# Kernel optimization log

Hardware: AMD Instinct MI355X
Metric: run time of the kernel (lower is better)

The kernel has to match this reference:

```python
import jax, jax.numpy as jnp
import numpy as np

R_S, R_C, P, L, NVOX, CH = 48, 144, 27, 2, 128, 128


def encode(x, L=L):
    # NeRF-style positional encoding: [sin(2^l x), cos(2^l x)] for l in range(L)
    feats = []
    for l in range(L):
        f = (2.0 ** l) * x
        feats.append(jnp.sin(f))
        feats.append(jnp.cos(f))
    return jnp.concatenate(feats, axis=-1)


def setup_inputs() -> dict:
    key = jax.random.key(0)
    ks = jax.random.split(key, 8)
    Np = 524288
    xyz = jax.random.uniform(ks[0], (Np, 3), dtype=jnp.float32)          # inside bbox [0,1]^3
    directions = jax.random.normal(ks[1], (Np, 3), dtype=jnp.float32)
    # voxel grid buffer: linspace over bbox per axis -> (3, NVOX)
    voxel = jnp.stack([jnp.linspace(0.0, 1.0, NVOX)] * 3, axis=0).astype(jnp.float32)
    sigma = 0.1 * jax.random.normal(ks[2], (3, R_S, NVOX), dtype=jnp.float32)
    feature = 0.1 * jax.random.normal(ks[3], (3, R_C, NVOX), dtype=jnp.float32)
    B = jax.random.normal(ks[4], (R_C, P), dtype=jnp.float32)
    din = (P + 3) * L * 2  # 120
    W1 = jax.random.normal(ks[5], (din, CH), dtype=jnp.float32) / jnp.sqrt(din)
    b1 = jnp.zeros((CH,), jnp.float32)
    W2 = jax.random.normal(ks[6], (CH, CH), dtype=jnp.float32) / jnp.sqrt(CH)
    b2 = jnp.zeros((CH,), jnp.float32)
    W3 = jax.random.normal(ks[7], (CH, 3), dtype=jnp.float32) / jnp.sqrt(CH)
    b3 = jnp.zeros((3,), jnp.float32)
    return {"xyz": xyz, "directions": directions, "voxel": voxel, "sigma": sigma,
            "feature": feature, "B": B, "W1": W1, "b1": b1, "W2": W2, "b2": b2,
            "W3": W3, "b3": b3}


def reference(xyz, directions, voxel, sigma, feature, B, W1, b1, W2, b2, W3, b3):
    SIGMA_BIAS = -5.0
    x = xyz.T  # (3, Np)
    Nv = voxel.shape[1]
    # snap_to_voxels: per-axis searchsorted + clamp + gather of grid coords
    inds = jax.vmap(jnp.searchsorted)(voxel, x)           # (3, Np)
    il = jnp.clip(inds - 1, 0, Nv - 1)
    ir = jnp.clip(inds, 0, Nv - 1)
    vl = jnp.take_along_axis(voxel, il, axis=1)           # (3, Np)
    vr = jnp.take_along_axis(voxel, ir, axis=1)
    w = (x - vl) / (vr - vl + 1e-6)                       # (3, Np) lerp weights

    # density: gather (3,R_s,Np), lerp, prod over axes(xyz), sum over rank
    sl = jnp.take_along_axis(sigma, il[:, None, :], axis=2)
    sr = jnp.take_along_axis(sigma, ir[:, None, :], axis=2)
    s = sl + (sr - sl) * w[:, None, :]                    # (3, R_s, Np)
    sigmas = jnp.sum(jnp.prod(s, axis=0), axis=0)         # (Np,)
    sigmas = jax.nn.softplus(sigmas + SIGMA_BIAS)

    # features: same pattern on (3,R_c,Np), then small matmul with B
    fl = jnp.take_along_axis(feature, il[:, None, :], axis=2)
    fr = jnp.take_along_axis(feature, ir[:, None, :], axis=2)
    f = fl + (fr - fl) * w[:, None, :]                    # (3, R_c, Np)
    feats = jnp.einsum('rn,rp->np', jnp.prod(f, axis=0), B)  # (Np, P)

    h = jnp.concatenate([encode(feats, L), encode(directions, L)], axis=1)  # (Np, 120)
    h = jax.nn.leaky_relu(h @ W1 + b1, negative_slope=0.01)
    h = jax.nn.leaky_relu(h @ W2 + b2, negative_slope=0.01)
    rgb = jax.nn.sigmoid(h @ W3 + b3)                     # (Np, 3)
    return sigmas, rgb
```

## Files before the change

### kernel.cpp

```cpp
#include <hip/hip_runtime.h>
#include <cstdint>

constexpr int RS  = 48;
constexpr int RC  = 144;
constexpr int PP  = 27;
constexpr int NV  = 128;
constexpr int CHN = 128;

constexpr int SIG_E  = 0;
constexpr int FEAT_E = 24576;
constexpr int BF_E   = 86016;
constexpr int W1_E   = 91136;
constexpr int W2_E   = 107520;
constexpr int W3_E   = 123904;
constexpr int TOT_E  = 125952;

typedef __attribute__((ext_vector_type(8))) short short8;
typedef __attribute__((ext_vector_type(4))) float f32x4;
typedef __attribute__((ext_vector_type(2))) unsigned int u32x2;
typedef __attribute__((ext_vector_type(4))) unsigned int u32x4;

__device__ __forceinline__ short f2bf(float f) {
    unsigned int u = __builtin_bit_cast(unsigned int, f);
    u += 0x7fffu + ((u >> 16) & 1u);
    return (short)(u >> 16);
}
__device__ __forceinline__ float bfu(unsigned int u) {
    return __builtin_bit_cast(float, u);
}
__device__ __forceinline__ unsigned int pk2bf(float a, float b) {
    unsigned short ua = __builtin_bit_cast(unsigned short, (__bf16)a);
    unsigned short ub = __builtin_bit_cast(unsigned short, (__bf16)b);
    return (unsigned int)ua | ((unsigned int)ub << 16);
}

__global__ void prep_kernel(const float* __restrict__ sigma, const float* __restrict__ feature,
                            const float* __restrict__ Bm, const float* __restrict__ W1,
                            const float* __restrict__ W2, const float* __restrict__ W3,
                            short* __restrict__ ws) {
    int idx = blockIdx.x * 256 + threadIdx.x;
    if (idx >= TOT_E) return;
    float val = 0.f;
    if (idx < FEAT_E) {
        int a = idx / 8192, t = idx % 8192;
        int v = t / 64, r = t % 64;
        val = (r < RS) ? sigma[(a * RS + r) * NV + v] : 0.f;
    } else if (idx < BF_E) {
        int j = idx - FEAT_E;
        int a = j / 20480, t = j % 20480;
        int v = t / 160, r = t % 160;
        val = (r < RC) ? feature[(a * RC + r) * NV + v] : 0.f;
    } else if (idx < W1_E) {
        int j = idx - BF_E;
        int frag = j >> 9, li = (j >> 3) & 63, e = j & 7;
        int kt = frag >> 1, nt = frag & 1;
        int k = kt * 32 + (li >> 4) * 8 + e;
        int n = nt * 16 + (li & 15);
        val = (k < RC && n < PP) ? Bm[k * PP + n] : 0.f;
    } else if (idx < W2_E) {
        int j = idx - W1_E;
        int frag = j >> 9, li = (j >> 3) & 63, e = j & 7;
        int kt = frag >> 3, nt = frag & 7;
        int kn = kt * 32 + (li >> 4) * 8 + e;
        int n = nt * 16 + (li & 15);
        if (kn < 120) {
            int ko;
            if (kn < 108) { ko = (kn & 3) * PP + (kn >> 2); }
            else { int t2 = kn - 108; ko = 108 + (t2 & 3) * 3 + (t2 >> 2); }
            val = W1[ko * CHN + n];
        }
    } else if (idx < W3_E) {
        int j = idx - W2_E;
        int frag = j >> 9, li = (j >> 3) & 63, e = j & 7;
        int kt = frag >> 3, nt = frag & 7;
        int k = kt * 32 + (li >> 4) * 8 + e;
        int n = nt * 16 + (li & 15);
        val = W2[k * CHN + n];
    } else {
        int j = idx - W3_E;
        int frag = j >> 9, li = (j >> 3) & 63, e = j & 7;
        int kt = frag;
        int k = kt * 32 + (li >> 4) * 8 + e;
        int n = li & 15;
        val = (n < 3) ? W3[k * 3 + n] : 0.f;
    }
    ws[idx] = f2bf(val);
}

__device__ __forceinline__ void lerp8(const short* rl, int stride, float w, float* pr, bool first) {
    u32x4 Lo = *(const u32x4*)rl;
    u32x4 Hi = *(const u32x4*)(rl + stride);
#pragma unroll
    for (int d = 0; d < 4; ++d) {
        unsigned int lw = Lo[d], hw = Hi[d];
        float fl0 = bfu(lw << 16), fl1 = bfu(lw & 0xffff0000u);
        float fh0 = bfu(hw << 16), fh1 = bfu(hw & 0xffff0000u);
        float s0 = fmaf(fh0 - fl0, w, fl0);
        float s1 = fmaf(fh1 - fl1, w, fl1);
        if (first) { pr[2 * d] = s0; pr[2 * d + 1] = s1; }
        else       { pr[2 * d] *= s0; pr[2 * d + 1] *= s1; }
    }
}

__global__ __launch_bounds__(256, 8)
void tensorf_main(const float* __restrict__ xyz, const float* __restrict__ dird,
                  const float* __restrict__ voxel,
                  const float* __restrict__ b1, const float* __restrict__ b2,
                  const float* __restrict__ b3,
                  const short* __restrict__ ws, float* __restrict__ out, int Np) {
    __shared__ float voxs[3 * NV];
    __shared__ char  X[4 * 16 * 256];

    const int tid = threadIdx.x;
    const int wid = tid >> 6;
    const int lane = tid & 63;
    const int quad = lane >> 4, lane16 = lane & 15;
    const int wavebase = blockIdx.x * 64 + wid * 16;
    char* Xw = X + wid * 16 * 256;

    for (int i = tid; i < 3 * NV; i += 256) voxs[i] = voxel[i];
    __syncthreads();

    const short* SIGT  = ws + SIG_E;
    const short* FEATT = ws + FEAT_E;
    const short* BFr   = ws + BF_E;

    {
        const int p = wavebase + lane16;

        int ipb[3]; float we[3];
#pragma unroll
        for (int a = 0; a < 3; ++a) {
            float x = xyz[p * 3 + a];
            int ind = (int)ceilf(x * 127.f);
            ind = min(max(ind, 0), 128);
            while (ind > 0 && voxs[a * NV + ind - 1] >= x) --ind;
            while (ind < 128 && voxs[a * NV + ind] < x) ++ind;
            int il = min(max(ind - 1, 0), 127);
            int ir = min(ind, 127);
            float vl = voxs[a * NV + il], vr = voxs[a * NV + ir];
            float w = (x - vl) / (vr - vl + 1e-6f);
            we[a] = (il == 127) ? 1.f : w;
            ipb[a] = min(il, 126);
        }

        float sig = 0.f;
#pragma unroll
        for (int kt = 0; kt < 2; ++kt) {
            float pr[8];
#pragma unroll
            for (int a = 0; a < 3; ++a)
                lerp8(SIGT + (a * NV + ipb[a]) * 64 + kt * 32 + quad * 8, 64, we[a], pr, a == 0);
#pragma unroll
            for (int j = 0; j < 8; ++j) sig += pr[j];
        }
        sig += __shfl_xor(sig, 16);
        sig += __shfl_xor(sig, 32);
        if (lane < 16) out[p] = log1pf(expf(sig - 5.f));

        f32x4 acc0 = {0.f, 0.f, 0.f, 0.f}, acc1 = {0.f, 0.f, 0.f, 0.f};
#pragma unroll
        for (int kt = 0; kt < 5; ++kt) {
            float pr[8];
#pragma unroll
            for (int a = 0; a < 3; ++a)
                lerp8(FEATT + (a * NV + ipb[a]) * 160 + kt * 32 + quad * 8, 160, we[a], pr, a == 0);
            u32x4 uu;
#pragma unroll
            for (int d = 0; d < 4; ++d) uu[d] = pk2bf(pr[2 * d], pr[2 * d + 1]);
            short8 af = __builtin_bit_cast(short8, uu);
            short8 bf0 = *(const short8*)(BFr + ((kt * 2 + 0) * 64 + lane) * 8);
            short8 bf1 = *(const short8*)(BFr + ((kt * 2 + 1) * 64 + lane) * 8);
            acc0 = __builtin_amdgcn_mfma_f32_16x16x32_bf16(af, bf0, acc0, 0, 0, 0);
            acc1 = __builtin_amdgcn_mfma_f32_16x16x32_bf16(af, bf1, acc1, 0, 0, 0);
        }

#pragma unroll
        for (int nt = 0; nt < 2; ++nt) {
            int c = nt * 16 + lane16;
            f32x4 A = nt ? acc1 : acc0;
            if (c < PP) {
#pragma unroll
                for (int j = 0; j < 4; ++j) {
                    int row = quad * 4 + j;
                    float f = A[j];
                    float s1 = __sinf(f), c1 = __cosf(f);
                    float s2 = 2.f * s1 * c1;
                    float c2 = fmaf(-2.f * s1, s1, 1.f);
                    unsigned int w0 = pk2bf(s1, c1);
                    unsigned int w1 = pk2bf(s2, c2);
                    int byte = c * 8;
                    int chunk = byte >> 4, off = byte & 15;
                    *(u32x2*)(Xw + row * 256 + ((chunk ^ (row & 7)) << 4) + off) = u32x2{w0, w1};
                }
            }
        }
        {
            int row = lane16;
            if (quad < 3) {
                float d = dird[p * 3 + quad];
                float s1 = __sinf(d), c1 = __cosf(d);
                float s2 = 2.f * s1 * c1;
                float c2 = fmaf(-2.f * s1, s1, 1.f);
                unsigned int w0 = pk2bf(s1, c1);
                unsigned int w1 = pk2bf(s2, c2);
                int byte = 216 + 8 * quad;
                int chunk = byte >> 4, off = byte & 15;
                *(u32x2*)(Xw + row * 256 + ((chunk ^ (row & 7)) << 4) + off) = u32x2{w0, w1};
            } else {
                int addr = row * 256 + ((15 ^ (row & 7)) << 4);
                *(u32x4*)(Xw + addr) = u32x4{0u, 0u, 0u, 0u};
            }
        }
    }
    __syncthreads();

    const short* W1F = ws + W1_E;
    const short* W2F = ws + W2_E;
    const short* W3F = ws + W3_E;

#pragma unroll 1
    for (int layer = 0; layer < 2; ++layer) {
        const short* WF = layer ? W2F : W1F;
        const float* bb = layer ? b2 : b1;

        short8 af[4];
#pragma unroll
        for (int kt = 0; kt < 4; ++kt) {
            int row = lane16;
            int chunk = kt * 4 + quad;
            af[kt] = *(const short8*)(Xw + row * 256 + ((chunk ^ (row & 7)) << 4));
        }

#pragma unroll 1
        for (int nt = 0; nt < 8; ++nt) {
            short8 wf[4];
#pragma unroll
            for (int kt = 0; kt < 4; ++kt)
                wf[kt] = *(const short8*)(WF + ((kt * 8 + nt) * 64 + lane) * 8);
            f32x4 acc = {0.f, 0.f, 0.f, 0.f};
#pragma unroll
            for (int kt = 0; kt < 4; ++kt)
                acc = __builtin_amdgcn_mfma_f32_16x16x32_bf16(af[kt], wf[kt], acc, 0, 0, 0);

            float bvv = bb[nt * 16 + lane16];
#pragma unroll
            for (int j = 0; j < 4; ++j) {
                float v = acc[j] + bvv;
                v = fmaxf(v, 0.01f * v);
                int row = quad * 4 + j;
                int byte = (nt * 16 + lane16) * 2;
                int chunk = byte >> 4, off = byte & 15;
                *(short*)(Xw + row * 256 + ((chunk ^ (row & 7)) << 4) + off) =
                    (short)__builtin_bit_cast(unsigned short, (__bf16)v);
            }
        }
        __syncthreads();
    }

    {
        short8 af[4];
#pragma unroll
        for (int kt = 0; kt < 4; ++kt) {
            int row = lane16;
            int chunk = kt * 4 + quad;
            af[kt] = *(const short8*)(Xw + row * 256 + ((chunk ^ (row & 7)) << 4));
        }
        short8 wf3[4];
#pragma unroll
        for (int kt = 0; kt < 4; ++kt)
            wf3[kt] = *(const short8*)(W3F + (kt * 64 + lane) * 8);

        f32x4 acc3 = {0.f, 0.f, 0.f, 0.f};
#pragma unroll
        for (int kt = 0; kt < 4; ++kt)
            acc3 = __builtin_amdgcn_mfma_f32_16x16x32_bf16(af[kt], wf3[kt], acc3, 0, 0, 0);

        if (lane16 < 3) {
            float bvv = b3[lane16];
#pragma unroll
            for (int j = 0; j < 4; ++j) {
                float v = acc3[j] + bvv;
                float r = 1.f / (1.f + expf(-v));
                int row = quad * 4 + j;
                out[Np + (wavebase + row) * 3 + lane16] = r;
            }
        }
    }
}

extern "C" void kernel_launch(void* const* d_in, const int* in_sizes, int n_in,
                              void* d_out, int out_size, void* d_ws, size_t ws_size,
                              hipStream_t stream) {
    (void)n_in; (void)out_size; (void)ws_size;
    const float* xyz      = (const float*)d_in[0];
    const float* dird     = (const float*)d_in[1];
    const float* voxel    = (const float*)d_in[2];
    const float* sigma    = (const float*)d_in[3];
    const float* feature  = (const float*)d_in[4];
    const float* Bm       = (const float*)d_in[5];
    const float* W1       = (const float*)d_in[6];
    const float* b1       = (const float*)d_in[7];
    const float* W2       = (const float*)d_in[8];
    const float* b2       = (const float*)d_in[9];
    const float* W3       = (const float*)d_in[10];
    const float* b3       = (const float*)d_in[11];
    float* out = (float*)d_out;
    short* ws  = (short*)d_ws;

    const int Np = in_sizes[0] / 3;

    prep_kernel<<<(TOT_E + 255) / 256, 256, 0, stream>>>(sigma, feature, Bm, W1, W2, W3, ws);
    tensorf_main<<<Np / 64, 256, 0, stream>>>(xyz, dird, voxel, b1, b2, b3, ws, out, Np);
}
```

Before: 209.8 us.

## Store factor tables as fp32 (lo, hi-lo) pairs and drop LDS voxel copy

```diff
diff --git a/kernel.cpp b/kernel.cpp
--- a/kernel.cpp
+++ b/kernel.cpp
@@ -7,13 +7,14 @@
 constexpr int NV  = 128;
 constexpr int CHN = 128;
 
-constexpr int SIG_E  = 0;
-constexpr int FEAT_E = 24576;
-constexpr int BF_E   = 86016;
-constexpr int W1_E   = 91136;
-constexpr int W2_E   = 107520;
-constexpr int W3_E   = 123904;
-constexpr int TOT_E  = 125952;
+constexpr int SIGP  = 3 * NV * 64;
+constexpr int FEATP = 3 * NV * 160;
+constexpr int NPAIR = SIGP + FEATP;
+constexpr int FR_B  = 0;
+constexpr int FR_W1 = 5120;
+constexpr int FR_W2 = 21504;
+constexpr int FR_W3 = 37888;
+constexpr int FR_TOT = 39936;
 
 typedef __attribute__((ext_vector_type(8))) short short8;
 typedef __attribute__((ext_vector_type(4))) float f32x4;
@@ -25,40 +26,52 @@
     u += 0x7fffu + ((u >> 16) & 1u);
     return (short)(u >> 16);
 }
-__device__ __forceinline__ float bfu(unsigned int u) {
-    return __builtin_bit_cast(float, u);
-}
 __device__ __forceinline__ unsigned int pk2bf(float a, float b) {
     unsigned short ua = __builtin_bit_cast(unsigned short, (__bf16)a);
     unsigned short ub = __builtin_bit_cast(unsigned short, (__bf16)b);
     return (unsigned int)ua | ((unsigned int)ub << 16);
 }
 
-__global__ void prep_kernel(const float* __restrict__ sigma, const float* __restrict__ feature,
-                            const float* __restrict__ Bm, const float* __restrict__ W1,
-                            const float* __restrict__ W2, const float* __restrict__ W3,
-                            short* __restrict__ ws) {
+__global__ void prep_tables(const float* __restrict__ sigma, const float* __restrict__ feature,
+                            float* __restrict__ wf) {
     int idx = blockIdx.x * 256 + threadIdx.x;
-    if (idx >= TOT_E) return;
-    float val = 0.f;
-    if (idx < FEAT_E) {
+    if (idx >= NPAIR) return;
+    float lo = 0.f, hi = 0.f;
+    if (idx < SIGP) {
         int a = idx / 8192, t = idx % 8192;
         int v = t / 64, r = t % 64;
-        val = (r < RS) ? sigma[(a * RS + r) * NV + v] : 0.f;
-    } else if (idx < BF_E) {
-        int j = idx - FEAT_E;
+        if (r < RS) {
+            lo = sigma[(a * RS + r) * NV + v];
+            hi = sigma[(a * RS + r) * NV + min(v + 1, NV - 1)];
+        }
+    } else {
+        int j = idx - SIGP;
         int a = j / 20480, t = j % 20480;
         int v = t / 160, r = t % 160;
-        val = (r < RC) ? feature[(a * RC + r) * NV + v] : 0.f;
-    } else if (idx < W1_E) {
-        int j = idx - BF_E;
+        if (r < RC) {
+            lo = feature[(a * RC + r) * NV + v];
+            hi = feature[(a * RC + r) * NV + min(v + 1, NV - 1)];
+        }
+    }
+    wf[2 * idx]     = lo;
+    wf[2 * idx + 1] = hi - lo;
+}
+
+__global__ void prep_frags(const float* __restrict__ Bm, const float* __restrict__ W1,
+                           const float* __restrict__ W2, const float* __restrict__ W3,
+                           short* __restrict__ fr) {
+    int idx = blockIdx.x * 256 + threadIdx.x;
+    if (idx >= FR_TOT) return;
+    float val = 0.f;
+    if (idx < FR_W1) {
+        int j = idx - FR_B;
         int frag = j >> 9, li = (j >> 3) & 63, e = j & 7;
         int kt = frag >> 1, nt = frag & 1;
         int k = kt * 32 + (li >> 4) * 8 + e;
         int n = nt * 16 + (li & 15);
         val = (k < RC && n < PP) ? Bm[k * PP + n] : 0.f;
-    } else if (idx < W2_E) {
-        int j = idx - W1_E;
+    } else if (idx < FR_W2) {
+        int j = idx - FR_W1;
         int frag = j >> 9, li = (j >> 3) & 63, e = j & 7;
         int kt = frag >> 3, nt = frag & 7;
         int kn = kt * 32 + (li >> 4) * 8 + e;
@@ -69,47 +82,43 @@
             else { int t2 = kn - 108; ko = 108 + (t2 & 3) * 3 + (t2 >> 2); }
             val = W1[ko * CHN + n];
         }
-    } else if (idx < W3_E) {
-        int j = idx - W2_E;
+    } else if (idx < FR_W3) {
+        int j = idx - FR_W2;
         int frag = j >> 9, li = (j >> 3) & 63, e = j & 7;
         int kt = frag >> 3, nt = frag & 7;
         int k = kt * 32 + (li >> 4) * 8 + e;
         int n = nt * 16 + (li & 15);
         val = W2[k * CHN + n];
     } else {
-        int j = idx - W3_E;
+        int j = idx - FR_W3;
         int frag = j >> 9, li = (j >> 3) & 63, e = j & 7;
         int kt = frag;
         int k = kt * 32 + (li >> 4) * 8 + e;
         int n = li & 15;
         val = (n < 3) ? W3[k * 3 + n] : 0.f;
     }
-    ws[idx] = f2bf(val);
-}
-
-__device__ __forceinline__ void lerp8(const short* rl, int stride, float w, float* pr, bool first) {
-    u32x4 Lo = *(const u32x4*)rl;
-    u32x4 Hi = *(const u32x4*)(rl + stride);
-#pragma unroll
-    for (int d = 0; d < 4; ++d) {
-        unsigned int lw = Lo[d], hw = Hi[d];
-        float fl0 = bfu(lw << 16), fl1 = bfu(lw & 0xffff0000u);
-        float fh0 = bfu(hw << 16), fh1 = bfu(hw & 0xffff0000u);
-        float s0 = fmaf(fh0 - fl0, w, fl0);
-        float s1 = fmaf(fh1 - fl1, w, fl1);
-        if (first) { pr[2 * d] = s0; pr[2 * d + 1] = s1; }
-        else       { pr[2 * d] *= s0; pr[2 * d + 1] *= s1; }
-    }
-}
-
-__global__ __launch_bounds__(256, 8)
+    fr[idx] = f2bf(val);
+}
+
+__device__ __forceinline__ void lerpd8(const float* rl, float w, float* pr, bool first) {
+#pragma unroll
+    for (int h = 0; h < 4; ++h) {
+        f32x4 v = *(const f32x4*)(rl + h * 4);
+        float s0 = fmaf(v[1], w, v[0]);
+        float s1 = fmaf(v[3], w, v[2]);
+        if (first) { pr[2 * h] = s0; pr[2 * h + 1] = s1; }
+        else       { pr[2 * h] *= s0; pr[2 * h + 1] *= s1; }
+    }
+}
+
+__global__ __launch_bounds__(256, 6)
 void tensorf_main(const float* __restrict__ xyz, const float* __restrict__ dird,
                   const float* __restrict__ voxel,
                   const float* __restrict__ b1, const float* __restrict__ b2,
                   const float* __restrict__ b3,
-                  const short* __restrict__ ws, float* __restrict__ out, int Np) {
-    __shared__ float voxs[3 * NV];
-    __shared__ char  X[4 * 16 * 256];
+                  const float* __restrict__ wf, const short* __restrict__ fr,
+                  float* __restrict__ out, int Np) {
+    __shared__ char X[4 * 16 * 256];
 
     const int tid = threadIdx.x;
     const int wid = tid >> 6;
@@ -118,12 +127,9 @@
     const int wavebase = blockIdx.x * 64 + wid * 16;
     char* Xw = X + wid * 16 * 256;
 
-    for (int i = tid; i < 3 * NV; i += 256) voxs[i] = voxel[i];
-    __syncthreads();
-
-    const short* SIGT  = ws + SIG_E;
-    const short* FEATT = ws + FEAT_E;
-    const short* BFr   = ws + BF_E;
+    const float* SIGF  = wf;
+    const float* FEATF = wf + 2 * SIGP;
+    const short* BFr   = fr + FR_B;
 
     {
         const int p = wavebase + lane16;
@@ -131,14 +137,15 @@
         int ipb[3]; float we[3];
 #pragma unroll
         for (int a = 0; a < 3; ++a) {
+            const float* vax = voxel + a * NV;
             float x = xyz[p * 3 + a];
             int ind = (int)ceilf(x * 127.f);
             ind = min(max(ind, 0), 128);
-            while (ind > 0 && voxs[a * NV + ind - 1] >= x) --ind;
-            while (ind < 128 && voxs[a * NV + ind] < x) ++ind;
+            while (ind > 0 && vax[ind - 1] >= x) --ind;
+            while (ind < 128 && vax[ind] < x) ++ind;
             int il = min(max(ind - 1, 0), 127);
             int ir = min(ind, 127);
-            float vl = voxs[a * NV + il], vr = voxs[a * NV + ir];
+            float vl = vax[il], vr = vax[ir];
             float w = (x - vl) / (vr - vl + 1e-6f);
             we[a] = (il == 127) ? 1.f : w;
             ipb[a] = min(il, 126);
@@ -150,7 +157,7 @@
             float pr[8];
 #pragma unroll
             for (int a = 0; a < 3; ++a)
-                lerp8(SIGT + (a * NV + ipb[a]) * 64 + kt * 32 + quad * 8, 64, we[a], pr, a == 0);
+                lerpd8(SIGF + ((a * NV + ipb[a]) * 64 + kt * 32 + quad * 8) * 2, we[a], pr, a == 0);
 #pragma unroll
             for (int j = 0; j < 8; ++j) sig += pr[j];
         }
@@ -164,7 +171,7 @@
             float pr[8];
 #pragma unroll
             for (int a = 0; a < 3; ++a)
-                lerp8(FEATT + (a * NV + ipb[a]) * 160 + kt * 32 + quad * 8, 160, we[a], pr, a == 0);
+                lerpd8(FEATF + ((a * NV + ipb[a]) * 160 + kt * 32 + quad * 8) * 2, we[a], pr, a == 0);
             u32x4 uu;
 #pragma unroll
             for (int d = 0; d < 4; ++d) uu[d] = pk2bf(pr[2 * d], pr[2 * d + 1]);
@@ -215,9 +222,9 @@
     }
     __syncthreads();
 
-    const short* W1F = ws + W1_E;
-    const short* W2F = ws + W2_E;
-    const short* W3F = ws + W3_E;
+    const short* W1F = fr + FR_W1;
+    const short* W2F = fr + FR_W2;
+    const short* W3F = fr + FR_W3;
 
 #pragma unroll 1
     for (int layer = 0; layer < 2; ++layer) {
@@ -234,14 +241,14 @@
 
 #pragma unroll 1
         for (int nt = 0; nt < 8; ++nt) {
-            short8 wf[4];
+            short8 wfv[4];
 #pragma unroll
             for (int kt = 0; kt < 4; ++kt)
-                wf[kt] = *(const short8*)(WF + ((kt * 8 + nt) * 64 + lane) * 8);
+                wfv[kt] = *(const short8*)(WF + ((kt * 8 + nt) * 64 + lane) * 8);
             f32x4 acc = {0.f, 0.f, 0.f, 0.f};
 #pragma unroll
             for (int kt = 0; kt < 4; ++kt)
-                acc = __builtin_amdgcn_mfma_f32_16x16x32_bf16(af[kt], wf[kt], acc, 0, 0, 0);
+                acc = __builtin_amdgcn_mfma_f32_16x16x32_bf16(af[kt], wfv[kt], acc, 0, 0, 0);
 
             float bvv = bb[nt * 16 + lane16];
 #pragma unroll
@@ -306,10 +313,12 @@
     const float* W3       = (const float*)d_in[10];
     const float* b3       = (const float*)d_in[11];
     float* out = (float*)d_out;
-    short* ws  = (short*)d_ws;
+    float* wf  = (float*)d_ws;
+    short* frg = (short*)d_ws + 2 * 2 * NPAIR;
 
     const int Np = in_sizes[0] / 3;
 
-    prep_kernel<<<(TOT_E + 255) / 256, 256, 0, stream>>>(sigma, feature, Bm, W1, W2, W3, ws);
-    tensorf_main<<<Np / 64, 256, 0, stream>>>(xyz, dird, voxel, b1, b2, b3, ws, out, Np);
-}
+    prep_tables<<<(NPAIR + 255) / 256, 256, 0, stream>>>(sigma, feature, wf);
+    prep_frags<<<(FR_TOT + 255) / 256, 256, 0, stream>>>(Bm, W1, W2, W3, frg);
+    tensorf_main<<<Np / 64, 256, 0, stream>>>(xyz, dird, voxel, b1, b2, b3, wf, frg, out, Np);
+}
```

Result: slower. 394.3 us (+87.9%).
